# Kernel tuning notes

Measured on AMD Instinct MI355X. Metric: run time of the kernel, lower is better.

The kernel has to match this reference:

```python
import jax, jax.numpy as jnp
import numpy as np

B, T, D, E, H = 8, 2048, 1024, 8, 256
LN_EPS = 1e-5  # torch.nn.LayerNorm default


def setup_inputs() -> dict:
    key = jax.random.key(0)
    ks = jax.random.split(key, 4)
    return {
        "x": jax.random.normal(ks[0], (B, T, D), dtype=jnp.float32),
        "Wg": jax.random.normal(ks[1], (E, D), dtype=jnp.float32) * 0.02,
        "ln_scale": jnp.ones((E, D), dtype=jnp.float32),
        "ln_bias": jnp.zeros((E, D), dtype=jnp.float32),
        "W1": jax.random.normal(ks[2], (E, D, H), dtype=jnp.float32) * 0.02,
        "b1": jnp.zeros((E, H), dtype=jnp.float32),
        "W2": jax.random.normal(ks[3], (E, H, D), dtype=jnp.float32) * 0.02,
        "b2": jnp.zeros((E, D), dtype=jnp.float32),
    }


def reference(x, Wg, ln_scale, ln_bias, W1, b1, W2, b2):
    Bs, Ts, Ds = x.shape
    xt = x.reshape(Bs * Ts, Ds)                      # [N, D]
    logits = xt @ Wg.T                               # [N, E]
    # softmax is monotone, so argmax(softmax(logits)) == argmax(logits)
    top1 = jnp.argmax(logits, axis=-1)               # [N] int

    # LayerNorm normalization is expert-independent; compute once.
    mu = jnp.mean(xt, axis=-1, keepdims=True)
    var = jnp.mean(jnp.square(xt - mu), axis=-1, keepdims=True)
    xhat = (xt - mu) * jax.lax.rsqrt(var + LN_EPS)   # [N, D]

    n_experts = Wg.shape[0]

    def body(y, p):
        s_e, b_e, w1, bb1, w2, bb2, eid = p
        h = jax.nn.gelu((xhat * s_e + b_e) @ w1 + bb1, approximate=False)  # [N, H]
        out = h @ w2 + bb2                                                  # [N, D]
        mask = (top1 == eid)[:, None].astype(out.dtype)
        return y + mask * out, None

    y0 = jnp.zeros_like(xt)
    y, _ = jax.lax.scan(
        body, y0, (ln_scale, ln_bias, W1, b1, W2, b2, jnp.arange(n_experts))
    )
    # dropout p=0.0 is identity
    return y.reshape(Bs, Ts, Ds)
```

## Files before the change

kernel.cpp:

```cpp
#include <hip/hip_runtime.h>
#include <hip/hip_bf16.h>
#include <math.h>

#define N_TOK 16384
#define D_DIM 1024
#define E_NUM 8
#define H_DIM 256
#define LN_EPS 1e-5f

#define BM 128
#define BN 128
#define BN1 64
#define BK 32
#define MAXTILES (N_TOK / BM + E_NUM)
#define MP (MAXTILES * BM)

#define TPB_TOK 2

typedef __attribute__((ext_vector_type(8))) short bf16x8;
typedef __attribute__((ext_vector_type(4))) float f32x4;

__device__ __forceinline__ unsigned short f2bf(float f) {
  union { float f; unsigned u; } cv; cv.f = f;
  unsigned u = cv.u;
  u += 0x7fffu + ((u >> 16) & 1u);
  return (unsigned short)(u >> 16);
}

__device__ __forceinline__ void gl_lds16(const void* g, void* l) {
  __builtin_amdgcn_global_load_lds(
      (const __attribute__((address_space(1))) unsigned int*)g,
      (__attribute__((address_space(3))) unsigned int*)l, 16, 0, 0);
}

__global__ __launch_bounds__(256) void smoe_gate(
    const float* __restrict__ x, const float* __restrict__ wg,
    const float* __restrict__ ln_s, const float* __restrict__ ln_b,
    unsigned short* __restrict__ xhat, int* __restrict__ eid)
{
  int t0 = blockIdx.x * TPB_TOK;
  int tid = threadIdx.x;
  int lane = tid & 63, wave = tid >> 6;

  const float4* x4 = (const float4*)x;
  float4 v[TPB_TOK];
  float s[TPB_TOK], ss[TPB_TOK];
  double lg[TPB_TOK][E_NUM];
#pragma unroll
  for (int u = 0; u < TPB_TOK; u++) {
    v[u] = x4[(size_t)(t0 + u) * 256 + tid];
    s[u]  = v[u].x + v[u].y + v[u].z + v[u].w;
    ss[u] = v[u].x * v[u].x + v[u].y * v[u].y + v[u].z * v[u].z + v[u].w * v[u].w;
  }
  const float4* wg4 = (const float4*)wg;
#pragma unroll
  for (int e = 0; e < E_NUM; e++) {
    float4 w = wg4[e * 256 + tid];
#pragma unroll
    for (int u = 0; u < TPB_TOK; u++)
      lg[u][e] = (double)v[u].x * w.x + (double)v[u].y * w.y
               + (double)v[u].z * w.z + (double)v[u].w * w.w;
  }

  __shared__ double lred[TPB_TOK][4][64];
  __shared__ float  wst[TPB_TOK][4][2];
  __shared__ double etot[TPB_TOK][E_NUM];
  __shared__ float  stot[TPB_TOK][2];

#pragma unroll
  for (int u = 0; u < TPB_TOK; u++) {
    double a0, a1, a2, a3;
    {
      double p0 = __shfl_xor(lg[u][0], 1, 64), p1 = __shfl_xor(lg[u][1], 1, 64);
      double p2 = __shfl_xor(lg[u][2], 1, 64), p3 = __shfl_xor(lg[u][3], 1, 64);
      double p4 = __shfl_xor(lg[u][4], 1, 64), p5 = __shfl_xor(lg[u][5], 1, 64);
      double p6 = __shfl_xor(lg[u][6], 1, 64), p7 = __shfl_xor(lg[u][7], 1, 64);
      bool b = lane & 1;
      a0 = b ? lg[u][1] + p1 : lg[u][0] + p0;
      a1 = b ? lg[u][3] + p3 : lg[u][2] + p2;
      a2 = b ? lg[u][5] + p5 : lg[u][4] + p4;
      a3 = b ? lg[u][7] + p7 : lg[u][6] + p6;
    }
    double c0, c1;
    {
      double q0 = __shfl_xor(a0, 2, 64), q1 = __shfl_xor(a1, 2, 64);
      double q2 = __shfl_xor(a2, 2, 64), q3 = __shfl_xor(a3, 2, 64);
      bool b = (lane >> 1) & 1;
      c0 = b ? a1 + q1 : a0 + q0;
      c1 = b ? a3 + q3 : a2 + q2;
    }
    double c;
    {
      double r0 = __shfl_xor(c0, 4, 64), r1 = __shfl_xor(c1, 4, 64);
      bool b = (lane >> 2) & 1;
      c = b ? c1 + r1 : c0 + r0;
    }
    lred[u][wave][lane] = c;

    float sv = s[u], ssv = ss[u];
#pragma unroll
    for (int m = 1; m < 64; m <<= 1) {
      sv  += __shfl_xor(sv, m, 64);
      ssv += __shfl_xor(ssv, m, 64);
    }
    if (lane == 0) { wst[u][wave][0] = sv; wst[u][wave][1] = ssv; }
  }
  __syncthreads();

  if (wave < TPB_TOK) {
    int u = wave;
    double t = lred[u][0][lane] + lred[u][1][lane]
             + lred[u][2][lane] + lred[u][3][lane];
    t += __shfl_xor(t, 8, 64);
    t += __shfl_xor(t, 16, 64);
    t += __shfl_xor(t, 32, 64);
    if (lane < E_NUM) etot[u][lane] = t;
    if (lane == 0) {
      stot[u][0] = wst[u][0][0] + wst[u][1][0] + wst[u][2][0] + wst[u][3][0];
      stot[u][1] = wst[u][0][1] + wst[u][1][1] + wst[u][2][1] + wst[u][3][1];
    }
  }
  __syncthreads();

#pragma unroll
  for (int u = 0; u < TPB_TOK; u++) {
    double bestv = etot[u][0]; int best = 0;
#pragma unroll
    for (int e = 1; e < E_NUM; e++) {
      double t = etot[u][e];
      if (t > bestv) { bestv = t; best = e; }
    }
    float mean = stot[u][0] * (1.0f / (float)D_DIM);
    float var  = stot[u][1] * (1.0f / (float)D_DIM) - mean * mean;
    float rstd = 1.0f / sqrtf(var + LN_EPS);
    if (tid == 0) eid[t0 + u] = best;
    float4 sc = ((const float4*)(ln_s + (size_t)best * D_DIM))[tid];
    float4 bi = ((const float4*)(ln_b + (size_t)best * D_DIM))[tid];
    ushort4 o;
    o.x = f2bf((v[u].x - mean) * rstd * sc.x + bi.x);
    o.y = f2bf((v[u].y - mean) * rstd * sc.y + bi.y);
    o.z = f2bf((v[u].z - mean) * rstd * sc.z + bi.z);
    o.w = f2bf((v[u].w - mean) * rstd * sc.w + bi.w);
    ((ushort4*)(xhat + (size_t)(t0 + u) * D_DIM))[tid] = o;
  }
}

__global__ __launch_bounds__(1024) void smoe_route(
    const int* __restrict__ eid, int* __restrict__ texp, int* __restrict__ tokp)
{
  int tid = threadIdx.x;
  int lane = tid & 63, wave = tid >> 6;

  int cnt[E_NUM] = {};
  int ee[16];
#pragma unroll
  for (int j = 0; j < 16; j++) {
    int e = eid[j * 1024 + tid];
    ee[j] = e;
#pragma unroll
    for (int k = 0; k < E_NUM; k++) cnt[k] += (e == k);
  }
  int inc[E_NUM];
#pragma unroll
  for (int k = 0; k < E_NUM; k++) inc[k] = cnt[k];
#pragma unroll
  for (int m = 1; m < 64; m <<= 1) {
#pragma unroll
    for (int k = 0; k < E_NUM; k++) {
      int o = __shfl_up(inc[k], m, 64);
      if (lane >= m) inc[k] += o;
    }
  }
  __shared__ int wtot[16][E_NUM];
  __shared__ int wbase[16][E_NUM];
  __shared__ int ebase[E_NUM];
  __shared__ int ecnt[E_NUM];
  __shared__ int epad[E_NUM];
  if (lane == 63)
#pragma unroll
    for (int k = 0; k < E_NUM; k++) wtot[wave][k] = inc[k];
  __syncthreads();
  if (tid == 0) {
    int run[E_NUM] = {};
    for (int w = 0; w < 16; w++)
#pragma unroll
      for (int k = 0; k < E_NUM; k++) { wbase[w][k] = run[k]; run[k] += wtot[w][k]; }
    int b = 0, ti = 0;
    for (int k = 0; k < E_NUM; k++) {
      ecnt[k] = run[k];
      ebase[k] = b;
      int nt = (run[k] + BM - 1) / BM;
      for (int j = 0; j < nt; j++) texp[ti++] = k;
      epad[k] = nt * BM;
      b += nt * BM;
    }
    for (; ti < MAXTILES; ti++) texp[ti] = -1;
  }
  __syncthreads();
  int tb[E_NUM];
#pragma unroll
  for (int k = 0; k < E_NUM; k++) tb[k] = wbase[wave][k] + inc[k] - cnt[k];
  int run2[E_NUM] = {};
#pragma unroll
  for (int j = 0; j < 16; j++) {
    int e = ee[j];
    int r = 0;
#pragma unroll
    for (int k = 0; k < E_NUM; k++) {
      if (e == k) r = tb[k] + run2[k];
      run2[k] += (e == k);
    }
    tokp[ebase[e] + r] = j * 1024 + tid;
  }
#pragma unroll
  for (int k = 0; k < E_NUM; k++) {
    int s0 = ebase[k] + ecnt[k], n = epad[k] - ecnt[k];
    for (int i = tid; i < n; i += 1024) tokp[s0 + i] = -1;
  }
}

__global__ __launch_bounds__(256) void smoe_cvt(
    const float* __restrict__ in, unsigned short* __restrict__ out, int R, int C)
{
  int rt = R / 32, ct = C / 32;
  int bid = blockIdx.x;
  int e = bid / (rt * ct);
  int rem = bid % (rt * ct);
  int r0 = (rem / ct) * 32, c0 = (rem % ct) * 32;
  __shared__ float tile[32][33];
  int tx = threadIdx.x & 31, ty = threadIdx.x >> 5;
  const float* src = in + (size_t)e * R * C;
#pragma unroll
  for (int i = 0; i < 4; i++)
    tile[ty + 8 * i][tx] = src[(size_t)(r0 + ty + 8 * i) * C + c0 + tx];
  __syncthreads();
  unsigned short* dst = out + (size_t)e * R * C;
#pragma unroll
  for (int i = 0; i < 4; i++)
    dst[(size_t)(c0 + ty + 8 * i) * R + r0 + tx] = f2bf(tile[tx][ty + 8 * i]);
}

__global__ __launch_bounds__(256) void smoe_gemm1(
    const unsigned short* __restrict__ xhat,
    const unsigned short* __restrict__ w1t,
    const float* __restrict__ b1,
    const int* __restrict__ texp,
    const int* __restrict__ tokp,
    unsigned short* __restrict__ hbuf)
{
  int mt = blockIdx.x;
  int e = texp[mt];
  if (e < 0) return;
  int nt = blockIdx.y;
  int tid = threadIdx.x;
  __shared__ unsigned short As[BM * BK];
  __shared__ unsigned short Bs[BN1 * BK];
  int r = tid >> 2;
  int c = tid & 3;
  int row0 = mt * BM + r, row1 = row0 + 64;
  int tok0 = tokp[row0]; tok0 = tok0 < 0 ? 0 : tok0;
  int tok1 = tokp[row1]; tok1 = tok1 < 0 ? 0 : tok1;
  const unsigned short* a0 = xhat + (size_t)tok0 * D_DIM + c * 8;
  const unsigned short* a1 = xhat + (size_t)tok1 * D_DIM + c * 8;
  const unsigned short* bb = w1t + (size_t)e * H_DIM * D_DIM
                           + (size_t)(nt * BN1 + r) * D_DIM + c * 8;
  unsigned short* As0 = As + r * BK + c * 8;
  unsigned short* As1 = As + (r + 64) * BK + c * 8;
  unsigned short* Bs0 = Bs + r * BK + c * 8;

  int wave = tid >> 6, lane = tid & 63;
  int wr = (wave >> 1) * 64;
  int wc = (wave & 1) * 32;
  int qm = lane & 15;
  int quad = lane >> 4;
  f32x4 acc[4][2] = {};

  for (int k0 = 0; k0 < D_DIM; k0 += BK) {
    gl_lds16(a0 + k0, As0);
    gl_lds16(a1 + k0, As1);
    gl_lds16(bb + k0, Bs0);
    __syncthreads();
    bf16x8 af[4], bf[2];
#pragma unroll
    for (int i = 0; i < 4; i++)
      af[i] = *(const bf16x8*)(As + (wr + i * 16 + qm) * BK + quad * 8);
#pragma unroll
    for (int i = 0; i < 2; i++)
      bf[i] = *(const bf16x8*)(Bs + (wc + i * 16 + qm) * BK + quad * 8);
#pragma unroll
    for (int mi = 0; mi < 4; mi++)
#pragma unroll
      for (int ni = 0; ni < 2; ni++)
        acc[mi][ni] = __builtin_amdgcn_mfma_f32_16x16x32_bf16(
            af[mi], bf[ni], acc[mi][ni], 0, 0, 0);
    __syncthreads();
  }
  int mbase = mt * BM;
#pragma unroll
  for (int ni = 0; ni < 2; ni++) {
    int col = nt * BN1 + wc + ni * 16 + qm;
    float bias = b1[e * H_DIM + col];
#pragma unroll
    for (int mi = 0; mi < 4; mi++) {
      int rl = wr + mi * 16 + quad * 4;
#pragma unroll
      for (int i = 0; i < 4; i++) {
        float vv = acc[mi][ni][i] + bias;
        float g = 0.5f * vv * (1.0f + erff(vv * 0.70710678118654752f));
        hbuf[(size_t)(mbase + rl + i) * H_DIM + col] = f2bf(g);
      }
    }
  }
}

__global__ __launch_bounds__(256) void smoe_gemm2(
    const unsigned short* __restrict__ hbuf,
    const unsigned short* __restrict__ w2t,
    const float* __restrict__ b2,
    const int* __restrict__ texp,
    const int* __restrict__ tokp,
    float* __restrict__ y)
{
  int mt = blockIdx.x;
  int e = texp[mt];
  if (e < 0) return;
  int nt = blockIdx.y;
  int tid = threadIdx.x;
  __shared__ unsigned short As[BM * BK];
  __shared__ unsigned short Bs[BN * BK];
  int r = tid >> 2;
  int c = tid & 3;
  const unsigned short* a0 = hbuf + (size_t)(mt * BM + r) * H_DIM + c * 8;
  const unsigned short* a1 = a0 + (size_t)64 * H_DIM;
  const unsigned short* bb = w2t + (size_t)e * D_DIM * H_DIM
                           + (size_t)(nt * BN + r) * H_DIM + c * 8;
  const unsigned short* bb1 = bb + (size_t)64 * H_DIM;
  unsigned short* As0 = As + r * BK + c * 8;
  unsigned short* As1 = As + (r + 64) * BK + c * 8;
  unsigned short* Bs0 = Bs + r * BK + c * 8;
  unsigned short* Bs1 = Bs + (r + 64) * BK + c * 8;

  int wave = tid >> 6, lane = tid & 63;
  int wr = (wave >> 1) * 64;
  int wc = (wave & 1) * 64;
  int qm = lane & 15;
  int quad = lane >> 4;
  f32x4 acc[4][4] = {};

  for (int k0 = 0; k0 < H_DIM; k0 += BK) {
    gl_lds16(a0 + k0, As0);
    gl_lds16(a1 + k0, As1);
    gl_lds16(bb + k0, Bs0);
    gl_lds16(bb1 + k0, Bs1);
    __syncthreads();
    bf16x8 af[4], bf[4];
#pragma unroll
    for (int i = 0; i < 4; i++) {
      af[i] = *(const bf16x8*)(As + (wr + i * 16 + qm) * BK + quad * 8);
      bf[i] = *(const bf16x8*)(Bs + (wc + i * 16 + qm) * BK + quad * 8);
    }
#pragma unroll
    for (int mi = 0; mi < 4; mi++)
#pragma unroll
      for (int ni = 0; ni < 4; ni++)
        acc[mi][ni] = __builtin_amdgcn_mfma_f32_16x16x32_bf16(
            af[mi], bf[ni], acc[mi][ni], 0, 0, 0);
    __syncthreads();
  }
  int mbase = mt * BM;
#pragma unroll
  for (int mi = 0; mi < 4; mi++) {
#pragma unroll
    for (int i = 0; i < 4; i++) {
      int row = mbase + wr + mi * 16 + quad * 4 + i;
      int tok = tokp[row];
      if (tok < 0) continue;
#pragma unroll
      for (int ni = 0; ni < 4; ni++) {
        int col = nt * BN + wc + ni * 16 + qm;
        y[(size_t)tok * D_DIM + col] = acc[mi][ni][i] + b2[e * D_DIM + col];
      }
    }
  }
}

extern "C" void kernel_launch(void* const* d_in, const int* in_sizes, int n_in,
                              void* d_out, int out_size, void* d_ws, size_t ws_size,
                              hipStream_t stream) {
  (void)in_sizes; (void)n_in; (void)out_size; (void)ws_size;
  const float* x    = (const float*)d_in[0];
  const float* wg   = (const float*)d_in[1];
  const float* ln_s = (const float*)d_in[2];
  const float* ln_b = (const float*)d_in[3];
  const float* w1   = (const float*)d_in[4];
  const float* b1   = (const float*)d_in[5];
  const float* w2   = (const float*)d_in[6];
  const float* b2   = (const float*)d_in[7];
  float* y = (float*)d_out;

  char* ws = (char*)d_ws;
  size_t off = 0;
  auto alloc = [&](size_t bytes) {
    void* p = ws + off;
    off = (off + bytes + 255) & ~(size_t)255;
    return p;
  };
  unsigned short* xhat = (unsigned short*)alloc((size_t)N_TOK * D_DIM * 2);
  unsigned short* w1t  = (unsigned short*)alloc((size_t)E_NUM * D_DIM * H_DIM * 2);
  unsigned short* w2t  = (unsigned short*)alloc((size_t)E_NUM * D_DIM * H_DIM * 2);
  unsigned short* hbuf = (unsigned short*)alloc((size_t)MP * H_DIM * 2);
  int* eid    = (int*)alloc((size_t)N_TOK * 4);
  int* tokp   = (int*)alloc((size_t)MP * 4);
  int* texp   = (int*)alloc((size_t)MAXTILES * 4);

  smoe_gate<<<N_TOK / TPB_TOK, 256, 0, stream>>>(x, wg, ln_s, ln_b, xhat, eid);
  smoe_route<<<1, 1024, 0, stream>>>(eid, texp, tokp);
  smoe_cvt<<<E_NUM * (D_DIM / 32) * (H_DIM / 32), 256, 0, stream>>>(w1, w1t, D_DIM, H_DIM);
  smoe_cvt<<<E_NUM * (H_DIM / 32) * (D_DIM / 32), 256, 0, stream>>>(w2, w2t, H_DIM, D_DIM);
  smoe_gemm1<<<dim3(MAXTILES, H_DIM / BN1), 256, 0, stream>>>(xhat, w1t, b1, texp, tokp, hbuf);
  smoe_gemm2<<<dim3(MAXTILES, D_DIM / BN), 256, 0, stream>>>(hbuf, w2t, b2, texp, tokp, y);
}
```

Baseline: 258.4 us.

## Use one wave per token in gate kernel and merge weight conversion launches

The gate/LayerNorm kernel now assigns each token to a single wavefront (four tokens per block), so all logit, mean and variance reductions and the top-1 argmax are done with wave shuffles instead of shared memory and two block barriers. The two weight transpose/convert launches are merged into one kernel that picks W1 or W2 by block index, saving one launch. The gate kernel gets fewer barriers and LDS traffic but more serial per-lane work and more loads per thread. Ties in the argmax go to the lower index, as before.

New measurement: 252.9 us. 1.02x faster.

```diff
diff --git a/kernel.cpp b/kernel.cpp
--- a/kernel.cpp
+++ b/kernel.cpp
@@ -15,8 +15,6 @@
 #define MAXTILES (N_TOK / BM + E_NUM)
 #define MP (MAXTILES * BM)
 
-#define TPB_TOK 2
-
 typedef __attribute__((ext_vector_type(8))) short bf16x8;
 typedef __attribute__((ext_vector_type(4))) float f32x4;
 
@@ -38,110 +36,94 @@
     const float* __restrict__ ln_s, const float* __restrict__ ln_b,
     unsigned short* __restrict__ xhat, int* __restrict__ eid)
 {
-  int t0 = blockIdx.x * TPB_TOK;
-  int tid = threadIdx.x;
-  int lane = tid & 63, wave = tid >> 6;
-
-  const float4* x4 = (const float4*)x;
-  float4 v[TPB_TOK];
-  float s[TPB_TOK], ss[TPB_TOK];
-  double lg[TPB_TOK][E_NUM];
-#pragma unroll
-  for (int u = 0; u < TPB_TOK; u++) {
-    v[u] = x4[(size_t)(t0 + u) * 256 + tid];
-    s[u]  = v[u].x + v[u].y + v[u].z + v[u].w;
-    ss[u] = v[u].x * v[u].x + v[u].y * v[u].y + v[u].z * v[u].z + v[u].w * v[u].w;
+  int lane = threadIdx.x & 63, wave = threadIdx.x >> 6;
+  int t = blockIdx.x * 4 + wave;
+
+  const float4* x4 = (const float4*)x + (size_t)t * 256;
+  float4 v[4];
+  float s = 0.f, ss = 0.f;
+#pragma unroll
+  for (int j = 0; j < 4; j++) {
+    v[j] = x4[lane + 64 * j];
+    s  += v[j].x + v[j].y + v[j].z + v[j].w;
+    ss += v[j].x * v[j].x + v[j].y * v[j].y + v[j].z * v[j].z + v[j].w * v[j].w;
   }
   const float4* wg4 = (const float4*)wg;
+  double lg[E_NUM];
 #pragma unroll
   for (int e = 0; e < E_NUM; e++) {
-    float4 w = wg4[e * 256 + tid];
-#pragma unroll
-    for (int u = 0; u < TPB_TOK; u++)
-      lg[u][e] = (double)v[u].x * w.x + (double)v[u].y * w.y
-               + (double)v[u].z * w.z + (double)v[u].w * w.w;
-  }
-
-  __shared__ double lred[TPB_TOK][4][64];
-  __shared__ float  wst[TPB_TOK][4][2];
-  __shared__ double etot[TPB_TOK][E_NUM];
-  __shared__ float  stot[TPB_TOK][2];
-
-#pragma unroll
-  for (int u = 0; u < TPB_TOK; u++) {
-    double a0, a1, a2, a3;
-    {
-      double p0 = __shfl_xor(lg[u][0], 1, 64), p1 = __shfl_xor(lg[u][1], 1, 64);
-      double p2 = __shfl_xor(lg[u][2], 1, 64), p3 = __shfl_xor(lg[u][3], 1, 64);
-      double p4 = __shfl_xor(lg[u][4], 1, 64), p5 = __shfl_xor(lg[u][5], 1, 64);
-      double p6 = __shfl_xor(lg[u][6], 1, 64), p7 = __shfl_xor(lg[u][7], 1, 64);
-      bool b = lane & 1;
-      a0 = b ? lg[u][1] + p1 : lg[u][0] + p0;
-      a1 = b ? lg[u][3] + p3 : lg[u][2] + p2;
-      a2 = b ? lg[u][5] + p5 : lg[u][4] + p4;
-      a3 = b ? lg[u][7] + p7 : lg[u][6] + p6;
-    }
-    double c0, c1;
-    {
-      double q0 = __shfl_xor(a0, 2, 64), q1 = __shfl_xor(a1, 2, 64);
-      double q2 = __shfl_xor(a2, 2, 64), q3 = __shfl_xor(a3, 2, 64);
-      bool b = (lane >> 1) & 1;
-      c0 = b ? a1 + q1 : a0 + q0;
-      c1 = b ? a3 + q3 : a2 + q2;
-    }
-    double c;
-    {
-      double r0 = __shfl_xor(c0, 4, 64), r1 = __shfl_xor(c1, 4, 64);
-      bool b = (lane >> 2) & 1;
-      c = b ? c1 + r1 : c0 + r0;
-    }
-    lred[u][wave][lane] = c;
-
-    float sv = s[u], ssv = ss[u];
-#pragma unroll
-    for (int m = 1; m < 64; m <<= 1) {
-      sv  += __shfl_xor(sv, m, 64);
-      ssv += __shfl_xor(ssv, m, 64);
-    }
-    if (lane == 0) { wst[u][wave][0] = sv; wst[u][wave][1] = ssv; }
-  }
-  __syncthreads();
-
-  if (wave < TPB_TOK) {
-    int u = wave;
-    double t = lred[u][0][lane] + lred[u][1][lane]
-             + lred[u][2][lane] + lred[u][3][lane];
-    t += __shfl_xor(t, 8, 64);
-    t += __shfl_xor(t, 16, 64);
-    t += __shfl_xor(t, 32, 64);
-    if (lane < E_NUM) etot[u][lane] = t;
-    if (lane == 0) {
-      stot[u][0] = wst[u][0][0] + wst[u][1][0] + wst[u][2][0] + wst[u][3][0];
-      stot[u][1] = wst[u][0][1] + wst[u][1][1] + wst[u][2][1] + wst[u][3][1];
-    }
-  }
-  __syncthreads();
-
-#pragma unroll
-  for (int u = 0; u < TPB_TOK; u++) {
-    double bestv = etot[u][0]; int best = 0;
-#pragma unroll
-    for (int e = 1; e < E_NUM; e++) {
-      double t = etot[u][e];
-      if (t > bestv) { bestv = t; best = e; }
-    }
-    float mean = stot[u][0] * (1.0f / (float)D_DIM);
-    float var  = stot[u][1] * (1.0f / (float)D_DIM) - mean * mean;
-    float rstd = 1.0f / sqrtf(var + LN_EPS);
-    if (tid == 0) eid[t0 + u] = best;
-    float4 sc = ((const float4*)(ln_s + (size_t)best * D_DIM))[tid];
-    float4 bi = ((const float4*)(ln_b + (size_t)best * D_DIM))[tid];
+    double acc = 0.0;
+#pragma unroll
+    for (int j = 0; j < 4; j++) {
+      float4 w = wg4[e * 256 + lane + 64 * j];
+      acc += (double)v[j].x * w.x + (double)v[j].y * w.y
+           + (double)v[j].z * w.z + (double)v[j].w * w.w;
+    }
+    lg[e] = acc;
+  }
+
+  double a0, a1, a2, a3;
+  {
+    double p0 = __shfl_xor(lg[0], 1, 64), p1 = __shfl_xor(lg[1], 1, 64);
+    double p2 = __shfl_xor(lg[2], 1, 64), p3 = __shfl_xor(lg[3], 1, 64);
+    double p4 = __shfl_xor(lg[4], 1, 64), p5 = __shfl_xor(lg[5], 1, 64);
+    double p6 = __shfl_xor(lg[6], 1, 64), p7 = __shfl_xor(lg[7], 1, 64);
+    bool b = lane & 1;
+    a0 = b ? lg[1] + p1 : lg[0] + p0;
+    a1 = b ? lg[3] + p3 : lg[2] + p2;
+    a2 = b ? lg[5] + p5 : lg[4] + p4;
+    a3 = b ? lg[7] + p7 : lg[6] + p6;
+  }
+  double c0, c1;
+  {
+    double q0 = __shfl_xor(a0, 2, 64), q1 = __shfl_xor(a1, 2, 64);
+    double q2 = __shfl_xor(a2, 2, 64), q3 = __shfl_xor(a3, 2, 64);
+    bool b = (lane >> 1) & 1;
+    c0 = b ? a1 + q1 : a0 + q0;
+    c1 = b ? a3 + q3 : a2 + q2;
+  }
+  double c;
+  {
+    double r0 = __shfl_xor(c0, 4, 64), r1 = __shfl_xor(c1, 4, 64);
+    bool b = (lane >> 2) & 1;
+    c = b ? c1 + r1 : c0 + r0;
+  }
+  c += __shfl_xor(c, 8, 64);
+  c += __shfl_xor(c, 16, 64);
+  c += __shfl_xor(c, 32, 64);
+
+  double val = c; int idx = lane & 7;
+#pragma unroll
+  for (int m = 1; m < E_NUM; m <<= 1) {
+    double ov = __shfl_xor(val, m, 64);
+    int    oi = __shfl_xor(idx, m, 64);
+    if (ov > val || (ov == val && oi < idx)) { val = ov; idx = oi; }
+  }
+  int best = idx;
+
+#pragma unroll
+  for (int m = 1; m < 64; m <<= 1) {
+    s  += __shfl_xor(s, m, 64);
+    ss += __shfl_xor(ss, m, 64);
+  }
+  float mean = s * (1.0f / (float)D_DIM);
+  float var  = ss * (1.0f / (float)D_DIM) - mean * mean;
+  float rstd = 1.0f / sqrtf(var + LN_EPS);
+
+  if (lane == 0) eid[t] = best;
+
+  const float4* s4 = (const float4*)(ln_s + (size_t)best * D_DIM);
+  const float4* b4 = (const float4*)(ln_b + (size_t)best * D_DIM);
+  ushort4* xo = (ushort4*)(xhat + (size_t)t * D_DIM);
+#pragma unroll
+  for (int j = 0; j < 4; j++) {
+    float4 sc = s4[lane + 64 * j], bi = b4[lane + 64 * j];
     ushort4 o;
-    o.x = f2bf((v[u].x - mean) * rstd * sc.x + bi.x);
-    o.y = f2bf((v[u].y - mean) * rstd * sc.y + bi.y);
-    o.z = f2bf((v[u].z - mean) * rstd * sc.z + bi.z);
-    o.w = f2bf((v[u].w - mean) * rstd * sc.w + bi.w);
-    ((ushort4*)(xhat + (size_t)(t0 + u) * D_DIM))[tid] = o;
+    o.x = f2bf((v[j].x - mean) * rstd * sc.x + bi.x);
+    o.y = f2bf((v[j].y - mean) * rstd * sc.y + bi.y);
+    o.z = f2bf((v[j].z - mean) * rstd * sc.z + bi.z);
+    o.w = f2bf((v[j].w - mean) * rstd * sc.w + bi.w);
+    xo[lane + 64 * j] = o;
   }
 }
 
@@ -219,11 +201,15 @@
   }
 }
 
-__global__ __launch_bounds__(256) void smoe_cvt(
-    const float* __restrict__ in, unsigned short* __restrict__ out, int R, int C)
+__global__ __launch_bounds__(256) void smoe_cvt2(
+    const float* __restrict__ w1, unsigned short* __restrict__ w1t,
+    const float* __restrict__ w2, unsigned short* __restrict__ w2t)
 {
+  int bid = blockIdx.x;
+  const float* in; unsigned short* out; int R, C;
+  if (bid < 2048) { in = w1; out = w1t; R = D_DIM; C = H_DIM; }
+  else            { in = w2; out = w2t; R = H_DIM; C = D_DIM; bid -= 2048; }
   int rt = R / 32, ct = C / 32;
-  int bid = blockIdx.x;
   int e = bid / (rt * ct);
   int rem = bid % (rt * ct);
   int r0 = (rem / ct) * 32, c0 = (rem % ct) * 32;
@@ -413,10 +399,9 @@
   int* tokp   = (int*)alloc((size_t)MP * 4);
   int* texp   = (int*)alloc((size_t)MAXTILES * 4);
 
-  smoe_gate<<<N_TOK / TPB_TOK, 256, 0, stream>>>(x, wg, ln_s, ln_b, xhat, eid);
+  smoe_gate<<<N_TOK / 4, 256, 0, stream>>>(x, wg, ln_s, ln_b, xhat, eid);
   smoe_route<<<1, 1024, 0, stream>>>(eid, texp, tokp);
-  smoe_cvt<<<E_NUM * (D_DIM / 32) * (H_DIM / 32), 256, 0, stream>>>(w1, w1t, D_DIM, H_DIM);
-  smoe_cvt<<<E_NUM * (H_DIM / 32) * (D_DIM / 32), 256, 0, stream>>>(w2, w2t, H_DIM, D_DIM);
+  smoe_cvt2<<<4096, 256, 0, stream>>>(w1, w1t, w2, w2t);
   smoe_gemm1<<<dim3(MAXTILES, H_DIM / BN1), 256, 0, stream>>>(xhat, w1t, b1, texp, tokp, hbuf);
   smoe_gemm2<<<dim3(MAXTILES, D_DIM / BN), 256, 0, stream>>>(hbuf, w2t, b2, texp, tokp, y);
 }
```
